# Kernel optimization log

Measured on AMD Instinct MI355X. Metric: run time of the kernel, lower is better.

Reference implementation:

```python
import jax, jax.numpy as jnp
import numpy as np

N_NODES = 50000
N_EDGES = 800000
N_GRAPHS = 512
EPS = 1e-5
SLOPE = 0.2  # LeakyReLU negative slope in GATv2


def setup_inputs() -> dict:
    key = jax.random.key(0)
    ks = jax.random.split(key, 20)
    s = 0.1
    inp = {
        "x": jax.random.normal(ks[0], (N_NODES, 9), jnp.float32),
        "edge_attr": jax.random.normal(ks[1], (N_EDGES, 3), jnp.float32),
        "Wl0": jax.random.normal(ks[2], (9, 64), jnp.float32) * s,
        "Wr0": jax.random.normal(ks[3], (9, 64), jnp.float32) * s,
        "bl0": jnp.zeros((64,), jnp.float32),
        "br0": jnp.zeros((64,), jnp.float32),
        "We0": jax.random.normal(ks[4], (3, 64), jnp.float32) * s,
        "att0": jax.random.normal(ks[5], (64,), jnp.float32) * s,
        "bo0": jnp.zeros((64,), jnp.float32),
        "Wl": jax.random.normal(ks[6], (4, 64, 64), jnp.float32) * s,
        "Wr": jax.random.normal(ks[7], (4, 64, 64), jnp.float32) * s,
        "bl": jnp.zeros((4, 64), jnp.float32),
        "br": jnp.zeros((4, 64), jnp.float32),
        "We": jax.random.normal(ks[8], (4, 3, 64), jnp.float32) * s,
        "att": jax.random.normal(ks[9], (4, 64), jnp.float32) * s,
        "bo": jnp.zeros((4, 64), jnp.float32),
        "bn_g": jnp.ones((5, 64), jnp.float32),
        "bn_b": jnp.zeros((5, 64), jnp.float32),
        "bn_m": jnp.zeros((5, 64), jnp.float32),
        "bn_v": jax.random.uniform(ks[10], (5, 64), jnp.float32, 0.5, 1.5),
        "Wjk": jax.random.normal(ks[11], (64, 64), jnp.float32) * s,
        "bjk": jnp.zeros((64,), jnp.float32),
        "Whead": jax.random.normal(ks[12], (64, 1), jnp.float32) * s,
        "bhead": jnp.zeros((1,), jnp.float32),
        "edge_index": jax.random.randint(ks[13], (2, N_EDGES), 0, N_NODES, jnp.int32),
        "batch": jnp.sort(jax.random.randint(ks[14], (N_NODES,), 0, N_GRAPHS, jnp.int32)),
        "num_graphs": N_GRAPHS,
    }
    return inp


def gatv2_layer(h, src, dst, ea, Wl_, bl_, Wr_, br_, We_, a_, bo_, n_nodes):
    # GATv2Conv (heads=1, edge_dim) : e_ij = a . LeakyReLU(Wl h_j + Wr h_i + We e_ij)
    xl = h @ Wl_ + bl_                          # [N, 64] source transform
    xr = h @ Wr_ + br_                          # [N, 64] dest transform
    e = jax.nn.leaky_relu(xl[src] + xr[dst] + ea @ We_, SLOPE)  # [E, 64]
    logit = e @ a_                              # [E]
    m = jax.ops.segment_max(logit, dst, num_segments=n_nodes)
    m = jnp.where(jnp.isfinite(m), m, 0.0)      # empty segments -> -inf
    p = jnp.exp(logit - m[dst])
    z = jax.ops.segment_sum(p, dst, num_segments=n_nodes)
    alpha = p / jnp.maximum(z[dst], 1e-16)      # softmax over in-edges of dst
    out = jax.ops.segment_sum(alpha[:, None] * xl[src], dst, num_segments=n_nodes)
    return out + bo_


def bn_relu(h, g, b, m, v):
    # eval-mode BatchNorm1d followed by ReLU (BasicGNN: norm then act)
    return jax.nn.relu((h - m) * (g * jax.lax.rsqrt(v + EPS)) + b)


def reference(x, edge_attr, Wl0, Wr0, bl0, br0, We0, att0, bo0,
              Wl, Wr, bl, br, We, att, bo,
              bn_g, bn_b, bn_m, bn_v, Wjk, bjk, Whead, bhead,
              edge_index, batch, num_graphs):
    n = x.shape[0]
    src, dst = edge_index[0], edge_index[1]
    h = gatv2_layer(x, src, dst, edge_attr, Wl0, bl0, Wr0, br0, We0, att0, bo0, n)
    h = bn_relu(h, bn_g[0], bn_b[0], bn_m[0], bn_v[0])
    for i in range(4):
        h = gatv2_layer(h, src, dst, edge_attr, Wl[i], bl[i], Wr[i], br[i], We[i], att[i], bo[i], n)
        h = bn_relu(h, bn_g[i + 1], bn_b[i + 1], bn_m[i + 1], bn_v[i + 1])
    h = h @ Wjk + bjk                            # jk='last' output projection 64->64
    # global mean pool over graphs
    sums = jax.ops.segment_sum(h, batch, num_segments=num_graphs)          # [G, 64]
    cnt = jax.ops.segment_sum(jnp.ones((n,), h.dtype), batch, num_segments=num_graphs)
    pooled = sums / jnp.maximum(cnt, 1.0)[:, None]
    return pooled @ Whead + bhead                # [G, 1]  (dropout inactive in eval)
```

## Files before the change

### kernel.cpp

```cpp
#include <hip/hip_runtime.h>
#include <math.h>

#define N_NODES 50000
#define N_EDGES 800000
#define N_GRAPHS 512
#define SLOPE 0.2f
#define CAP 48
static constexpr float EPS_BN = 1e-5f;

typedef float v2f __attribute__((ext_vector_type(2)));


__global__ __launch_bounds__(256) void scatter_t9_kernel(
    const int* __restrict__ src, const int* __restrict__ dst,
    const float* __restrict__ ea,
    int* __restrict__ cnt, float4* __restrict__ rec,
    const float* __restrict__ x,
    const float* __restrict__ Wl0, const float* __restrict__ bl0,
    const float* __restrict__ Wr0, const float* __restrict__ br0,
    float* __restrict__ xl, float* __restrict__ xr) {
    int t = threadIdx.x;
    int e = blockIdx.x * 256 + t;
    if (e < N_EDGES) {
        int d = dst[e];
        int pos = atomicAdd(&cnt[d], 1);
        if (pos < CAP)
            rec[(size_t)d * CAP + pos] = make_float4(__int_as_float(src[e] * 64),
                                                     ea[e * 3 + 0], ea[e * 3 + 1], ea[e * 3 + 2]);
    }

    int w = t >> 6;
    int k = t & 63;
    v2f wlr[9];
#pragma unroll
    for (int j = 0; j < 9; j++) wlr[j] = (v2f){Wl0[j * 64 + k], Wr0[j * 64 + k]};
    v2f bias = {bl0[k], br0[k]};
    const int NW = gridDim.x * 4;
    for (int n = blockIdx.x * 4 + w; n < N_NODES; n += NW) {
        int un = __builtin_amdgcn_readfirstlane(n);
        const float* __restrict__ hrow = x + (size_t)un * 9;
        float hb[9];
#pragma unroll
        for (int j = 0; j < 9; j++) hb[j] = hrow[j];
        v2f acc = bias;
#pragma unroll
        for (int j = 0; j < 9; j++)
            acc = __builtin_elementwise_fma((v2f){hb[j], hb[j]}, wlr[j], acc);
        xl[(size_t)un * 64 + k] = acc.x;
        xr[(size_t)un * 64 + k] = acc.y;
    }
}


__global__ __launch_bounds__(256) void transform5_kernel(
    const float* __restrict__ h,
    const float* __restrict__ Wl, const float* __restrict__ bl,
    const float* __restrict__ Wr, const float* __restrict__ br,
    float* __restrict__ xl, float* __restrict__ xr) {
    __shared__ float sAt[64][68];
    __shared__ float sB[64][128];
    int t = threadIdx.x;
    int n0 = blockIdx.x * 64;

#pragma unroll
    for (int i = 0; i < 4; i++) {
        int idx = i * 256 + t;
        int row = idx >> 4;
        int fc  = idx & 15;
        int n = n0 + row;
        float4 v = (n < N_NODES) ? *((const float4*)(h + (size_t)n * 64 + fc * 4))
                                 : make_float4(0.f, 0.f, 0.f, 0.f);
        sAt[fc * 4 + 0][row] = v.x;
        sAt[fc * 4 + 1][row] = v.y;
        sAt[fc * 4 + 2][row] = v.z;
        sAt[fc * 4 + 3][row] = v.w;
    }
#pragma unroll
    for (int i = 0; i < 8; i++) {
        int idx = i * 256 + t;
        int j  = idx >> 5;
        int fc = idx & 31;
        int c  = fc * 4;
        float4 v = (c < 64) ? *((const float4*)(Wl + j * 64 + c))
                            : *((const float4*)(Wr + j * 64 + (c - 64)));
        *((float4*)&sB[j][c]) = v;
    }
    __syncthreads();

    int tx = t & 15, ty = t >> 4;
    int col0 = tx * 8;
    const float* bsrc = (col0 < 64) ? (bl + col0) : (br + (col0 - 64));
    v2f acc[4][4];
#pragma unroll
    for (int r = 0; r < 4; r++)
#pragma unroll
        for (int cc = 0; cc < 4; cc++)
            acc[r][cc] = (v2f){bsrc[cc * 2], bsrc[cc * 2 + 1]};

#pragma unroll 4
    for (int j = 0; j < 64; j++) {
        float a0 = sAt[j][ty * 4 + 0];
        float a1 = sAt[j][ty * 4 + 1];
        float a2 = sAt[j][ty * 4 + 2];
        float a3 = sAt[j][ty * 4 + 3];
        float4 bq0 = *((const float4*)&sB[j][col0]);
        float4 bq1 = *((const float4*)&sB[j][col0 + 4]);
        v2f b0 = {bq0.x, bq0.y}, b1 = {bq0.z, bq0.w};
        v2f b2 = {bq1.x, bq1.y}, b3 = {bq1.z, bq1.w};
        v2f a0v = {a0, a0}, a1v = {a1, a1}, a2v = {a2, a2}, a3v = {a3, a3};
        acc[0][0] = __builtin_elementwise_fma(a0v, b0, acc[0][0]);
        acc[0][1] = __builtin_elementwise_fma(a0v, b1, acc[0][1]);
        acc[0][2] = __builtin_elementwise_fma(a0v, b2, acc[0][2]);
        acc[0][3] = __builtin_elementwise_fma(a0v, b3, acc[0][3]);
        acc[1][0] = __builtin_elementwise_fma(a1v, b0, acc[1][0]);
        acc[1][1] = __builtin_elementwise_fma(a1v, b1, acc[1][1]);
        acc[1][2] = __builtin_elementwise_fma(a1v, b2, acc[1][2]);
        acc[1][3] = __builtin_elementwise_fma(a1v, b3, acc[1][3]);
        acc[2][0] = __builtin_elementwise_fma(a2v, b0, acc[2][0]);
        acc[2][1] = __builtin_elementwise_fma(a2v, b1, acc[2][1]);
        acc[2][2] = __builtin_elementwise_fma(a2v, b2, acc[2][2]);
        acc[2][3] = __builtin_elementwise_fma(a2v, b3, acc[2][3]);
        acc[3][0] = __builtin_elementwise_fma(a3v, b0, acc[3][0]);
        acc[3][1] = __builtin_elementwise_fma(a3v, b1, acc[3][1]);
        acc[3][2] = __builtin_elementwise_fma(a3v, b2, acc[3][2]);
        acc[3][3] = __builtin_elementwise_fma(a3v, b3, acc[3][3]);
    }

#pragma unroll
    for (int r = 0; r < 4; r++) {
        int n = n0 + ty * 4 + r;
        if (n < N_NODES) {
            float4 lo = make_float4(acc[r][0].x, acc[r][0].y, acc[r][1].x, acc[r][1].y);
            float4 hi = make_float4(acc[r][2].x, acc[r][2].y, acc[r][3].x, acc[r][3].y);
            float* dstp = (col0 < 64) ? (xl + (size_t)n * 64 + col0)
                                      : (xr + (size_t)n * 64 + (col0 - 64));
            *((float4*)dstp) = lo;
            *((float4*)(dstp + 4)) = hi;
        }
    }
}


#define GAT_BODY(MASKED)                                                             \
    {                                                                                \
        int pA = c + q;                                                              \
        int pB = c + 4 + q;                                                          \
        bool vA = true, vB = true;                                                   \
        if (MASKED) {                                                                \
            vA = pA < end; if (!vA) pA = beg;                                        \
            vB = pB < end; if (!vB) pB = beg;                                        \
        }                                                                            \
        float4 rA = recP[pA];                                                        \
        float4 rB = recP[pB];                                                        \
        unsigned offA = (unsigned)__float_as_int(rA.x) + k4;                         \
        unsigned offB = (unsigned)__float_as_int(rB.x) + k4;                         \
        float4 xA = *(const float4*)(xl + offA);                                     \
        float4 xB = *(const float4*)(xl + offB);                                     \
        v2f xAa = {xA.x, xA.y}, xAb = {xA.z, xA.w};                                  \
        v2f xBa = {xB.x, xB.y}, xBb = {xB.z, xB.w};                                  \
        v2f tAa = xAa + xra, tAb = xAb + xrb;                                        \
        v2f tBa = xBa + xra, tBb = xBb + xrb;                                        \
        tAa = __builtin_elementwise_fma((v2f){rA.y, rA.y}, we0a, tAa);               \
        tAb = __builtin_elementwise_fma((v2f){rA.y, rA.y}, we0b, tAb);               \
        tBa = __builtin_elementwise_fma((v2f){rB.y, rB.y}, we0a, tBa);               \
        tBb = __builtin_elementwise_fma((v2f){rB.y, rB.y}, we0b, tBb);               \
        tAa = __builtin_elementwise_fma((v2f){rA.z, rA.z}, we1a, tAa);               \
        tAb = __builtin_elementwise_fma((v2f){rA.z, rA.z}, we1b, tAb);               \
        tBa = __builtin_elementwise_fma((v2f){rB.z, rB.z}, we1a, tBa);               \
        tBb = __builtin_elementwise_fma((v2f){rB.z, rB.z}, we1b, tBb);               \
        tAa = __builtin_elementwise_fma((v2f){rA.w, rA.w}, we2a, tAa);               \
        tAb = __builtin_elementwise_fma((v2f){rA.w, rA.w}, we2b, tAb);               \
        tBa = __builtin_elementwise_fma((v2f){rB.w, rB.w}, we2a, tBa);               \
        tBb = __builtin_elementwise_fma((v2f){rB.w, rB.w}, we2b, tBb);               \
        tAa = __builtin_elementwise_max(tAa, tAa * SLOPE);                           \
        tAb = __builtin_elementwise_max(tAb, tAb * SLOPE);                           \
        tBa = __builtin_elementwise_max(tBa, tBa * SLOPE);                           \
        tBb = __builtin_elementwise_max(tBb, tBb * SLOPE);                           \
        v2f dA = ata * tAa; dA = __builtin_elementwise_fma(atb, tAb, dA);            \
        v2f dB = ata * tBa; dB = __builtin_elementwise_fma(atb, tBb, dB);            \
        float accA = dA.x + dA.y;                                                    \
        float accB = dB.x + dB.y;                                                    \
        accA += __shfl_xor(accA, 1, 64);  accB += __shfl_xor(accB, 1, 64);           \
        accA += __shfl_xor(accA, 2, 64);  accB += __shfl_xor(accB, 2, 64);           \
        accA += __shfl_xor(accA, 4, 64);  accB += __shfl_xor(accB, 4, 64);           \
        accA += __shfl_xor(accA, 8, 64);  accB += __shfl_xor(accB, 8, 64);           \
        float peA = __expf(accA);                                                    \
        float peB = __expf(accB);                                                    \
        if (MASKED) { peA = vA ? peA : 0.f; peB = vB ? peB : 0.f; }                  \
        v2f pA2 = {peA, peA}, pB2 = {peB, peB};                                      \
        oAa = __builtin_elementwise_fma(pA2, xAa, oAa);                              \
        oAb = __builtin_elementwise_fma(pA2, xAb, oAb);                              \
        oBa = __builtin_elementwise_fma(pB2, xBa, oBa);                              \
        oBb = __builtin_elementwise_fma(pB2, xBb, oBb);                              \
        zA += peA; zB += peB;                                                        \
    }

__global__ __launch_bounds__(256) void gat_fused8_kernel(
    const float* __restrict__ xl, const float* __restrict__ xr,
    const float4* __restrict__ recP, const int* __restrict__ cnt,
    const float* __restrict__ We, const float* __restrict__ att,
    const float* __restrict__ bo,
    const float* __restrict__ bn_g, const float* __restrict__ bn_b,
    const float* __restrict__ bn_m, const float* __restrict__ bn_v,
    float* __restrict__ hout) {
    int t = threadIdx.x;
    int w = t >> 6;
    int lane = t & 63;
    int q = lane >> 4;
    int r = lane & 15;
    int k4 = r * 4;

    float4 we0 = *(const float4*)(We + 0 * 64 + k4);
    float4 we1 = *(const float4*)(We + 64 + k4);
    float4 we2 = *(const float4*)(We + 128 + k4);
    float4 at4 = *(const float4*)(att + k4);
    v2f we0a = {we0.x, we0.y}, we0b = {we0.z, we0.w};
    v2f we1a = {we1.x, we1.y}, we1b = {we1.z, we1.w};
    v2f we2a = {we2.x, we2.y}, we2b = {we2.z, we2.w};
    v2f ata  = {at4.x, at4.y}, atb  = {at4.z, at4.w};

    float4 g4  = *(const float4*)(bn_g + k4);
    float4 b4  = *(const float4*)(bn_b + k4);
    float4 m4  = *(const float4*)(bn_m + k4);
    float4 v4  = *(const float4*)(bn_v + k4);
    float4 bo4 = *(const float4*)(bo + k4);
    float Sx = g4.x * rsqrtf(v4.x + EPS_BN);
    float Sy = g4.y * rsqrtf(v4.y + EPS_BN);
    float Sz = g4.z * rsqrtf(v4.z + EPS_BN);
    float Sw = g4.w * rsqrtf(v4.w + EPS_BN);
    v2f Sa = {Sx, Sy}, Sb = {Sz, Sw};
    v2f Ta = {fmaf(bo4.x - m4.x, Sx, b4.x), fmaf(bo4.y - m4.y, Sy, b4.y)};
    v2f Tb = {fmaf(bo4.z - m4.z, Sz, b4.z), fmaf(bo4.w - m4.w, Sw, b4.w)};

    int n0 = blockIdx.x * 8 + w * 2;

#pragma unroll
    for (int nn = 0; nn < 2; nn++) {
        int n = n0 + nn;
        float4 xq = *(const float4*)(xr + (size_t)n * 64 + k4);
        v2f xra = {xq.x, xq.y}, xrb = {xq.z, xq.w};
        int deg = min(cnt[n], CAP);
        int beg = n * CAP;
        int end = beg + deg;
        int fullc = beg + (deg & ~7);

        v2f oAa = {0.f, 0.f}, oAb = {0.f, 0.f};
        v2f oBa = {0.f, 0.f}, oBb = {0.f, 0.f};
        float zA = 0.f, zB = 0.f;

        int c = beg;
        for (; c < fullc; c += 8) GAT_BODY(0)
        if (c < end) GAT_BODY(1)

        v2f oa = oAa + oBa, ob = oAb + oBb;
        float z = zA + zB;
        float4 o = make_float4(oa.x, oa.y, ob.x, ob.y);
        o.x += __shfl_xor(o.x, 16, 64); o.x += __shfl_xor(o.x, 32, 64);
        o.y += __shfl_xor(o.y, 16, 64); o.y += __shfl_xor(o.y, 32, 64);
        o.z += __shfl_xor(o.z, 16, 64); o.z += __shfl_xor(o.z, 32, 64);
        o.w += __shfl_xor(o.w, 16, 64); o.w += __shfl_xor(o.w, 32, 64);
        z += __shfl_xor(z, 16, 64); z += __shfl_xor(z, 32, 64);

        if (q == 0) {
            float zi = __builtin_amdgcn_rcpf(fmaxf(z, 1e-16f));
            v2f ra = {o.x * zi, o.y * zi};
            v2f rb = {o.z * zi, o.w * zi};
            ra = __builtin_elementwise_fma(ra, Sa, Ta);
            rb = __builtin_elementwise_fma(rb, Sb, Tb);
            ra = __builtin_elementwise_max(ra, (v2f){0.f, 0.f});
            rb = __builtin_elementwise_max(rb, (v2f){0.f, 0.f});
            float4 res = make_float4(ra.x, ra.y, rb.x, rb.y);
            *(float4*)(hout + (size_t)n * 64 + k4) = res;
        }
    }
}


__global__ __launch_bounds__(64) void pool_all_kernel(
    const float* __restrict__ h, const int* __restrict__ batch,
    const float* __restrict__ Wjk, const float* __restrict__ bjk,
    const float* __restrict__ Whead, const float* __restrict__ bhead,
    float* __restrict__ out) {
    int g = blockIdx.x;
    int k = threadIdx.x;
    int lo = 0, hi = N_NODES;
    while (lo < hi) { int mid = (lo + hi) >> 1; if (batch[mid] < g) lo = mid + 1; else hi = mid; }
    int s = lo;
    hi = N_NODES;
    while (lo < hi) { int mid = (lo + hi) >> 1; if (batch[mid] < g + 1) lo = mid + 1; else hi = mid; }
    int e = lo;

    float wc = 0.f;
    for (int j = 0; j < 64; j++) wc = fmaf(Wjk[k * 64 + j], Whead[j], wc);
    float bc = bjk[k] * Whead[k];
    for (int off = 32; off > 0; off >>= 1) bc += __shfl_xor(bc, off, 64);

    float acc = 0.f;
    for (int n = s; n < e; ++n) acc += h[(size_t)n * 64 + k];
    float cntf = (float)(e - s);
    acc /= fmaxf(cntf, 1.0f);
    float v = acc * wc;
    for (int off = 32; off > 0; off >>= 1) v += __shfl_xor(v, off, 64);
    if (k == 0) out[g] = v + bc + bhead[0];
}


extern "C" void kernel_launch(void* const* d_in, const int* in_sizes, int n_in,
                              void* d_out, int out_size, void* d_ws, size_t ws_size,
                              hipStream_t stream) {
    const float* x     = (const float*)d_in[0];
    const float* ea    = (const float*)d_in[1];
    const float* Wl0   = (const float*)d_in[2];
    const float* Wr0   = (const float*)d_in[3];
    const float* bl0   = (const float*)d_in[4];
    const float* br0   = (const float*)d_in[5];
    const float* We0   = (const float*)d_in[6];
    const float* att0  = (const float*)d_in[7];
    const float* bo0   = (const float*)d_in[8];
    const float* Wl    = (const float*)d_in[9];
    const float* Wr    = (const float*)d_in[10];
    const float* bl    = (const float*)d_in[11];
    const float* br    = (const float*)d_in[12];
    const float* We    = (const float*)d_in[13];
    const float* att   = (const float*)d_in[14];
    const float* bo    = (const float*)d_in[15];
    const float* bn_g  = (const float*)d_in[16];
    const float* bn_b  = (const float*)d_in[17];
    const float* bn_m  = (const float*)d_in[18];
    const float* bn_v  = (const float*)d_in[19];
    const float* Wjk   = (const float*)d_in[20];
    const float* bjk   = (const float*)d_in[21];
    const float* Whead = (const float*)d_in[22];
    const float* bhead = (const float*)d_in[23];
    const int* edge_index = (const int*)d_in[24];
    const int* batch      = (const int*)d_in[25];

    const int* srcIdx = edge_index;
    const int* dstIdx = edge_index + N_EDGES;

    char* ws = (char*)d_ws;
    size_t off = 0;
    auto alloc = [&](size_t bytes) -> void* {
        void* p = ws + off;
        off += (bytes + 255) & ~(size_t)255;
        return p;
    };
    float* hA      = (float*)alloc((size_t)N_NODES * 64 * 4);
    float* hB      = (float*)alloc((size_t)N_NODES * 64 * 4);
    float* xlb     = (float*)alloc((size_t)N_NODES * 64 * 4);
    float* xrb     = (float*)alloc((size_t)N_NODES * 64 * 4);
    int*   cnt     = (int*)alloc((size_t)N_NODES * 4);
    float4* recP   = (float4*)alloc((size_t)N_NODES * CAP * 16);

    hipMemsetAsync(cnt, 0, (size_t)N_NODES * 4, stream);
    scatter_t9_kernel<<<(N_EDGES + 255) / 256, 256, 0, stream>>>(
        srcIdx, dstIdx, ea, cnt, recP, x, Wl0, bl0, Wr0, br0, xlb, xrb);

    const int NBN2 = N_NODES / 8;
    const int NBG  = (N_NODES + 63) / 64;

    gat_fused8_kernel<<<NBN2, 256, 0, stream>>>(xlb, xrb, recP, cnt,
                                                We0, att0, bo0,
                                                bn_g, bn_b, bn_m, bn_v, hA);

    float* hcur = hA;
    float* hnext = hB;
    for (int i = 0; i < 4; i++) {
        transform5_kernel<<<NBG, 256, 0, stream>>>(hcur,
            Wl + (size_t)i * 64 * 64, bl + (size_t)i * 64,
            Wr + (size_t)i * 64 * 64, br + (size_t)i * 64,
            xlb, xrb);
        gat_fused8_kernel<<<NBN2, 256, 0, stream>>>(xlb, xrb, recP, cnt,
            We + (size_t)i * 3 * 64, att + (size_t)i * 64,
            bo + (size_t)i * 64,
            bn_g + (size_t)(i + 1) * 64, bn_b + (size_t)(i + 1) * 64,
            bn_m + (size_t)(i + 1) * 64, bn_v + (size_t)(i + 1) * 64,
            hnext);
        float* tp = hcur; hcur = hnext; hnext = tp;
    }

    pool_all_kernel<<<N_GRAPHS, 64, 0, stream>>>(hcur, batch, Wjk, bjk, Whead, bhead,
                                                 (float*)d_out);
}
```

Before: 531.3 us.

## Fuse GAT aggregation with next layer's linear transform in one kernel

Replaces the separate transform and GAT aggregation kernels with a layer-fused kernel. Each 1024-thread block aggregates 64 nodes, applies BN+ReLU into shared memory, then immediately computes the next layer's Wl/Wr projections, so the hidden state never round-trips through global memory. The masked tail loop is also merged into a single predicated loop, and BN scale/shift is recomputed with a division and sqrt instead of precomputed rsqrt constants. The risks are lower occupancy and more serialized work per block, since each wave processes four nodes sequentially in the 1024-thread blocks.

```diff
diff --git a/kernel.cpp b/kernel.cpp
--- a/kernel.cpp
+++ b/kernel.cpp
@@ -52,106 +52,15 @@
 }
 
 
-__global__ __launch_bounds__(256) void transform5_kernel(
-    const float* __restrict__ h,
-    const float* __restrict__ Wl, const float* __restrict__ bl,
-    const float* __restrict__ Wr, const float* __restrict__ br,
-    float* __restrict__ xl, float* __restrict__ xr) {
-    __shared__ float sAt[64][68];
-    __shared__ float sB[64][128];
-    int t = threadIdx.x;
-    int n0 = blockIdx.x * 64;
-
-#pragma unroll
-    for (int i = 0; i < 4; i++) {
-        int idx = i * 256 + t;
-        int row = idx >> 4;
-        int fc  = idx & 15;
-        int n = n0 + row;
-        float4 v = (n < N_NODES) ? *((const float4*)(h + (size_t)n * 64 + fc * 4))
-                                 : make_float4(0.f, 0.f, 0.f, 0.f);
-        sAt[fc * 4 + 0][row] = v.x;
-        sAt[fc * 4 + 1][row] = v.y;
-        sAt[fc * 4 + 2][row] = v.z;
-        sAt[fc * 4 + 3][row] = v.w;
-    }
-#pragma unroll
-    for (int i = 0; i < 8; i++) {
-        int idx = i * 256 + t;
-        int j  = idx >> 5;
-        int fc = idx & 31;
-        int c  = fc * 4;
-        float4 v = (c < 64) ? *((const float4*)(Wl + j * 64 + c))
-                            : *((const float4*)(Wr + j * 64 + (c - 64)));
-        *((float4*)&sB[j][c]) = v;
-    }
-    __syncthreads();
-
-    int tx = t & 15, ty = t >> 4;
-    int col0 = tx * 8;
-    const float* bsrc = (col0 < 64) ? (bl + col0) : (br + (col0 - 64));
-    v2f acc[4][4];
-#pragma unroll
-    for (int r = 0; r < 4; r++)
-#pragma unroll
-        for (int cc = 0; cc < 4; cc++)
-            acc[r][cc] = (v2f){bsrc[cc * 2], bsrc[cc * 2 + 1]};
-
-#pragma unroll 4
-    for (int j = 0; j < 64; j++) {
-        float a0 = sAt[j][ty * 4 + 0];
-        float a1 = sAt[j][ty * 4 + 1];
-        float a2 = sAt[j][ty * 4 + 2];
-        float a3 = sAt[j][ty * 4 + 3];
-        float4 bq0 = *((const float4*)&sB[j][col0]);
-        float4 bq1 = *((const float4*)&sB[j][col0 + 4]);
-        v2f b0 = {bq0.x, bq0.y}, b1 = {bq0.z, bq0.w};
-        v2f b2 = {bq1.x, bq1.y}, b3 = {bq1.z, bq1.w};
-        v2f a0v = {a0, a0}, a1v = {a1, a1}, a2v = {a2, a2}, a3v = {a3, a3};
-        acc[0][0] = __builtin_elementwise_fma(a0v, b0, acc[0][0]);
-        acc[0][1] = __builtin_elementwise_fma(a0v, b1, acc[0][1]);
-        acc[0][2] = __builtin_elementwise_fma(a0v, b2, acc[0][2]);
-        acc[0][3] = __builtin_elementwise_fma(a0v, b3, acc[0][3]);
-        acc[1][0] = __builtin_elementwise_fma(a1v, b0, acc[1][0]);
-        acc[1][1] = __builtin_elementwise_fma(a1v, b1, acc[1][1]);
-        acc[1][2] = __builtin_elementwise_fma(a1v, b2, acc[1][2]);
-        acc[1][3] = __builtin_elementwise_fma(a1v, b3, acc[1][3]);
-        acc[2][0] = __builtin_elementwise_fma(a2v, b0, acc[2][0]);
-        acc[2][1] = __builtin_elementwise_fma(a2v, b1, acc[2][1]);
-        acc[2][2] = __builtin_elementwise_fma(a2v, b2, acc[2][2]);
-        acc[2][3] = __builtin_elementwise_fma(a2v, b3, acc[2][3]);
-        acc[3][0] = __builtin_elementwise_fma(a3v, b0, acc[3][0]);
-        acc[3][1] = __builtin_elementwise_fma(a3v, b1, acc[3][1]);
-        acc[3][2] = __builtin_elementwise_fma(a3v, b2, acc[3][2]);
-        acc[3][3] = __builtin_elementwise_fma(a3v, b3, acc[3][3]);
-    }
-
-#pragma unroll
-    for (int r = 0; r < 4; r++) {
-        int n = n0 + ty * 4 + r;
-        if (n < N_NODES) {
-            float4 lo = make_float4(acc[r][0].x, acc[r][0].y, acc[r][1].x, acc[r][1].y);
-            float4 hi = make_float4(acc[r][2].x, acc[r][2].y, acc[r][3].x, acc[r][3].y);
-            float* dstp = (col0 < 64) ? (xl + (size_t)n * 64 + col0)
-                                      : (xr + (size_t)n * 64 + (col0 - 64));
-            *((float4*)dstp) = lo;
-            *((float4*)(dstp + 4)) = hi;
-        }
-    }
-}
-
-
-#define GAT_BODY(MASKED)                                                             \
-    {                                                                                \
-        int pA = c + q;                                                              \
-        int pB = c + 4 + q;                                                          \
-        bool vA = true, vB = true;                                                   \
-        if (MASKED) {                                                                \
-            vA = pA < end; if (!vA) pA = beg;                                        \
-            vB = pB < end; if (!vB) pB = beg;                                        \
-        }                                                                            \
-        float4 rA = recP[pA];                                                        \
-        float4 rB = recP[pB];                                                        \
+#define GAT_EDGE_LOOP()                                                              \
+    v2f oAa = {0.f, 0.f}, oAb = {0.f, 0.f};                                          \
+    v2f oBa = {0.f, 0.f}, oBb = {0.f, 0.f};                                          \
+    float zA = 0.f, zB = 0.f;                                                        \
+    for (int c = beg; c < end; c += 8) {                                             \
+        int pA = c + q;     bool vA = pA < end; int iA = vA ? pA : beg;              \
+        int pB = c + 4 + q; bool vB = pB < end; int iB = vB ? pB : beg;              \
+        float4 rA = recP[iA];                                                        \
+        float4 rB = recP[iB];                                                        \
         unsigned offA = (unsigned)__float_as_int(rA.x) + k4;                         \
         unsigned offB = (unsigned)__float_as_int(rB.x) + k4;                         \
         float4 xA = *(const float4*)(xl + offA);                                     \
@@ -184,18 +93,146 @@
         accA += __shfl_xor(accA, 2, 64);  accB += __shfl_xor(accB, 2, 64);           \
         accA += __shfl_xor(accA, 4, 64);  accB += __shfl_xor(accB, 4, 64);           \
         accA += __shfl_xor(accA, 8, 64);  accB += __shfl_xor(accB, 8, 64);           \
-        float peA = __expf(accA);                                                    \
-        float peB = __expf(accB);                                                    \
-        if (MASKED) { peA = vA ? peA : 0.f; peB = vB ? peB : 0.f; }                  \
+        float peA = vA ? __expf(accA) : 0.f;                                         \
+        float peB = vB ? __expf(accB) : 0.f;                                         \
         v2f pA2 = {peA, peA}, pB2 = {peB, peB};                                      \
         oAa = __builtin_elementwise_fma(pA2, xAa, oAa);                              \
         oAb = __builtin_elementwise_fma(pA2, xAb, oAb);                              \
         oBa = __builtin_elementwise_fma(pB2, xBa, oBa);                              \
         oBb = __builtin_elementwise_fma(pB2, xBb, oBb);                              \
         zA += peA; zB += peB;                                                        \
-    }
-
-__global__ __launch_bounds__(256) void gat_fused8_kernel(
+    }                                                                                \
+    v2f oa = oAa + oBa, ob = oAb + oBb;                                              \
+    float z = zA + zB;                                                               \
+    float4 o = make_float4(oa.x, oa.y, ob.x, ob.y);                                  \
+    o.x += __shfl_xor(o.x, 16, 64); o.x += __shfl_xor(o.x, 32, 64);                  \
+    o.y += __shfl_xor(o.y, 16, 64); o.y += __shfl_xor(o.y, 32, 64);                  \
+    o.z += __shfl_xor(o.z, 16, 64); o.z += __shfl_xor(o.z, 32, 64);                  \
+    o.w += __shfl_xor(o.w, 16, 64); o.w += __shfl_xor(o.w, 32, 64);                  \
+    z += __shfl_xor(z, 16, 64); z += __shfl_xor(z, 32, 64);
+
+#define GAT_PROLOGUE()                                                               \
+    float4 we0 = *(const float4*)(We + 0 * 64 + k4);                                 \
+    float4 we1 = *(const float4*)(We + 64 + k4);                                     \
+    float4 we2 = *(const float4*)(We + 128 + k4);                                    \
+    float4 at4 = *(const float4*)(att + k4);                                         \
+    v2f we0a = {we0.x, we0.y}, we0b = {we0.z, we0.w};                                \
+    v2f we1a = {we1.x, we1.y}, we1b = {we1.z, we1.w};                                \
+    v2f we2a = {we2.x, we2.y}, we2b = {we2.z, we2.w};                                \
+    v2f ata  = {at4.x, at4.y}, atb  = {at4.z, at4.w};                                \
+    float4 bo4 = *(const float4*)(bo + k4);                                          \
+    float4 g4  = *(const float4*)(bn_g + k4);                                        \
+    float4 b4  = *(const float4*)(bn_b + k4);                                        \
+    float4 m4  = *(const float4*)(bn_m + k4);                                        \
+    float4 v4  = *(const float4*)(bn_v + k4);
+
+#define GAT_BN_RES()                                                                 \
+    float zi = 1.0f / fmaxf(z, 1e-16f);                                              \
+    float4 res;                                                                      \
+    res.x = fmaxf((o.x * zi + bo4.x - m4.x) * (g4.x / sqrtf(v4.x + EPS_BN)) + b4.x, 0.f); \
+    res.y = fmaxf((o.y * zi + bo4.y - m4.y) * (g4.y / sqrtf(v4.y + EPS_BN)) + b4.y, 0.f); \
+    res.z = fmaxf((o.z * zi + bo4.z - m4.z) * (g4.z / sqrtf(v4.z + EPS_BN)) + b4.z, 0.f); \
+    res.w = fmaxf((o.w * zi + bo4.w - m4.w) * (g4.w / sqrtf(v4.w + EPS_BN)) + b4.w, 0.f);
+
+
+__global__ __launch_bounds__(1024) void layer_fused_kernel(
+    const float* __restrict__ xl, const float* __restrict__ xr,
+    const float4* __restrict__ recP, const int* __restrict__ cnt,
+    const float* __restrict__ We, const float* __restrict__ att,
+    const float* __restrict__ bo,
+    const float* __restrict__ bn_g, const float* __restrict__ bn_b,
+    const float* __restrict__ bn_m, const float* __restrict__ bn_v,
+    const float* __restrict__ Wl, const float* __restrict__ bl,
+    const float* __restrict__ Wr, const float* __restrict__ br,
+    float* __restrict__ xl_out, float* __restrict__ xr_out) {
+    __shared__ float sAt[64][65];
+    __shared__ float sB[64][128];
+    int t = threadIdx.x;
+    int n0 = blockIdx.x * 64;
+
+#pragma unroll
+    for (int i = 0; i < 2; i++) {
+        int idx = i * 1024 + t;
+        int j  = idx >> 5;
+        int fc = idx & 31;
+        int c  = fc * 4;
+        float4 v = (c < 64) ? *((const float4*)(Wl + j * 64 + c))
+                            : *((const float4*)(Wr + j * 64 + (c - 64)));
+        *((float4*)&sB[j][c]) = v;
+    }
+
+    int w = t >> 6;
+    int lane = t & 63;
+    int q = lane >> 4;
+    int r = lane & 15;
+    int k4 = r * 4;
+
+    GAT_PROLOGUE()
+
+#pragma unroll
+    for (int nn = 0; nn < 4; nn++) {
+        int nb = w * 4 + nn;
+        int n = n0 + nb;
+        if (n < N_NODES) {
+            float4 xq = *(const float4*)(xr + (size_t)n * 64 + k4);
+            v2f xra = {xq.x, xq.y}, xrb = {xq.z, xq.w};
+            int beg = n * CAP;
+            int end = beg + min(cnt[n], CAP);
+            GAT_EDGE_LOOP()
+            if (q == 0) {
+                GAT_BN_RES()
+                sAt[k4 + 0][nb] = res.x;
+                sAt[k4 + 1][nb] = res.y;
+                sAt[k4 + 2][nb] = res.z;
+                sAt[k4 + 3][nb] = res.w;
+            }
+        } else if (q == 0) {
+            sAt[k4 + 0][nb] = 0.f;
+            sAt[k4 + 1][nb] = 0.f;
+            sAt[k4 + 2][nb] = 0.f;
+            sAt[k4 + 3][nb] = 0.f;
+        }
+    }
+    __syncthreads();
+
+    int tx = t & 63;
+    int ty = t >> 6;
+    int col0 = tx * 2;
+    const float* bsrc = (col0 < 64) ? (bl + col0) : (br + (col0 - 64));
+    v2f bias = {bsrc[0], bsrc[1]};
+    v2f a0 = bias, a1 = bias, a2 = bias, a3 = bias;
+    int row0 = ty * 4;
+#pragma unroll 8
+    for (int j = 0; j < 64; j++) {
+        float h0 = sAt[j][row0 + 0];
+        float h1 = sAt[j][row0 + 1];
+        float h2 = sAt[j][row0 + 2];
+        float h3 = sAt[j][row0 + 3];
+        v2f b = *((const v2f*)&sB[j][col0]);
+        a0 = __builtin_elementwise_fma((v2f){h0, h0}, b, a0);
+        a1 = __builtin_elementwise_fma((v2f){h1, h1}, b, a1);
+        a2 = __builtin_elementwise_fma((v2f){h2, h2}, b, a2);
+        a3 = __builtin_elementwise_fma((v2f){h3, h3}, b, a3);
+    }
+    float* outbase = (col0 < 64) ? (xl_out + col0) : (xr_out + (col0 - 64));
+    {
+        int n = n0 + row0;
+        if (n + 3 < N_NODES) {
+            *((v2f*)(outbase + (size_t)(n + 0) * 64)) = a0;
+            *((v2f*)(outbase + (size_t)(n + 1) * 64)) = a1;
+            *((v2f*)(outbase + (size_t)(n + 2) * 64)) = a2;
+            *((v2f*)(outbase + (size_t)(n + 3) * 64)) = a3;
+        } else {
+            if (n + 0 < N_NODES) *((v2f*)(outbase + (size_t)(n + 0) * 64)) = a0;
+            if (n + 1 < N_NODES) *((v2f*)(outbase + (size_t)(n + 1) * 64)) = a1;
+            if (n + 2 < N_NODES) *((v2f*)(outbase + (size_t)(n + 2) * 64)) = a2;
+            if (n + 3 < N_NODES) *((v2f*)(outbase + (size_t)(n + 3) * 64)) = a3;
+        }
+    }
+}
+
+
+__global__ __launch_bounds__(256) void gat_final_kernel(
     const float* __restrict__ xl, const float* __restrict__ xr,
     const float4* __restrict__ recP, const int* __restrict__ cnt,
     const float* __restrict__ We, const float* __restrict__ att,
@@ -209,69 +246,17 @@
     int q = lane >> 4;
     int r = lane & 15;
     int k4 = r * 4;
-
-    float4 we0 = *(const float4*)(We + 0 * 64 + k4);
-    float4 we1 = *(const float4*)(We + 64 + k4);
-    float4 we2 = *(const float4*)(We + 128 + k4);
-    float4 at4 = *(const float4*)(att + k4);
-    v2f we0a = {we0.x, we0.y}, we0b = {we0.z, we0.w};
-    v2f we1a = {we1.x, we1.y}, we1b = {we1.z, we1.w};
-    v2f we2a = {we2.x, we2.y}, we2b = {we2.z, we2.w};
-    v2f ata  = {at4.x, at4.y}, atb  = {at4.z, at4.w};
-
-    float4 g4  = *(const float4*)(bn_g + k4);
-    float4 b4  = *(const float4*)(bn_b + k4);
-    float4 m4  = *(const float4*)(bn_m + k4);
-    float4 v4  = *(const float4*)(bn_v + k4);
-    float4 bo4 = *(const float4*)(bo + k4);
-    float Sx = g4.x * rsqrtf(v4.x + EPS_BN);
-    float Sy = g4.y * rsqrtf(v4.y + EPS_BN);
-    float Sz = g4.z * rsqrtf(v4.z + EPS_BN);
-    float Sw = g4.w * rsqrtf(v4.w + EPS_BN);
-    v2f Sa = {Sx, Sy}, Sb = {Sz, Sw};
-    v2f Ta = {fmaf(bo4.x - m4.x, Sx, b4.x), fmaf(bo4.y - m4.y, Sy, b4.y)};
-    v2f Tb = {fmaf(bo4.z - m4.z, Sz, b4.z), fmaf(bo4.w - m4.w, Sw, b4.w)};
-
-    int n0 = blockIdx.x * 8 + w * 2;
-
-#pragma unroll
-    for (int nn = 0; nn < 2; nn++) {
-        int n = n0 + nn;
-        float4 xq = *(const float4*)(xr + (size_t)n * 64 + k4);
-        v2f xra = {xq.x, xq.y}, xrb = {xq.z, xq.w};
-        int deg = min(cnt[n], CAP);
-        int beg = n * CAP;
-        int end = beg + deg;
-        int fullc = beg + (deg & ~7);
-
-        v2f oAa = {0.f, 0.f}, oAb = {0.f, 0.f};
-        v2f oBa = {0.f, 0.f}, oBb = {0.f, 0.f};
-        float zA = 0.f, zB = 0.f;
-
-        int c = beg;
-        for (; c < fullc; c += 8) GAT_BODY(0)
-        if (c < end) GAT_BODY(1)
-
-        v2f oa = oAa + oBa, ob = oAb + oBb;
-        float z = zA + zB;
-        float4 o = make_float4(oa.x, oa.y, ob.x, ob.y);
-        o.x += __shfl_xor(o.x, 16, 64); o.x += __shfl_xor(o.x, 32, 64);
-        o.y += __shfl_xor(o.y, 16, 64); o.y += __shfl_xor(o.y, 32, 64);
-        o.z += __shfl_xor(o.z, 16, 64); o.z += __shfl_xor(o.z, 32, 64);
-        o.w += __shfl_xor(o.w, 16, 64); o.w += __shfl_xor(o.w, 32, 64);
-        z += __shfl_xor(z, 16, 64); z += __shfl_xor(z, 32, 64);
-
-        if (q == 0) {
-            float zi = __builtin_amdgcn_rcpf(fmaxf(z, 1e-16f));
-            v2f ra = {o.x * zi, o.y * zi};
-            v2f rb = {o.z * zi, o.w * zi};
-            ra = __builtin_elementwise_fma(ra, Sa, Ta);
-            rb = __builtin_elementwise_fma(rb, Sb, Tb);
-            ra = __builtin_elementwise_max(ra, (v2f){0.f, 0.f});
-            rb = __builtin_elementwise_max(rb, (v2f){0.f, 0.f});
-            float4 res = make_float4(ra.x, ra.y, rb.x, rb.y);
-            *(float4*)(hout + (size_t)n * 64 + k4) = res;
-        }
+    int n = blockIdx.x * 4 + w;
+
+    GAT_PROLOGUE()
+    float4 xq = *(const float4*)(xr + (size_t)n * 64 + k4);
+    v2f xra = {xq.x, xq.y}, xrb = {xq.z, xq.w};
+    int beg = n * CAP;
+    int end = beg + min(cnt[n], CAP);
+    GAT_EDGE_LOOP()
+    if (q == 0) {
+        GAT_BN_RES()
+        *(float4*)(hout + (size_t)n * 64 + k4) = res;
     }
 }
 
@@ -345,40 +330,50 @@
         off += (bytes + 255) & ~(size_t)255;
         return p;
     };
-    float* hA      = (float*)alloc((size_t)N_NODES * 64 * 4);
-    float* hB      = (float*)alloc((size_t)N_NODES * 64 * 4);
-    float* xlb     = (float*)alloc((size_t)N_NODES * 64 * 4);
-    float* xrb     = (float*)alloc((size_t)N_NODES * 64 * 4);
+    float* xlA     = (float*)alloc((size_t)N_NODES * 64 * 4);
+    float* xrA     = (float*)alloc((size_t)N_NODES * 64 * 4);
+    float* xlB     = (float*)alloc((size_t)N_NODES * 64 * 4);
+    float* xrB     = (float*)alloc((size_t)N_NODES * 64 * 4);
+    float* hfin    = (float*)alloc((size_t)N_NODES * 64 * 4);
     int*   cnt     = (int*)alloc((size_t)N_NODES * 4);
     float4* recP   = (float4*)alloc((size_t)N_NODES * CAP * 16);
 
     hipMemsetAsync(cnt, 0, (size_t)N_NODES * 4, stream);
     scatter_t9_kernel<<<(N_EDGES + 255) / 256, 256, 0, stream>>>(
-        srcIdx, dstIdx, ea, cnt, recP, x, Wl0, bl0, Wr0, br0, xlb, xrb);
-
-    const int NBN2 = N_NODES / 8;
-    const int NBG  = (N_NODES + 63) / 64;
-
-    gat_fused8_kernel<<<NBN2, 256, 0, stream>>>(xlb, xrb, recP, cnt,
-                                                We0, att0, bo0,
-                                                bn_g, bn_b, bn_m, bn_v, hA);
-
-    float* hcur = hA;
-    float* hnext = hB;
-    for (int i = 0; i < 4; i++) {
-        transform5_kernel<<<NBG, 256, 0, stream>>>(hcur,
-            Wl + (size_t)i * 64 * 64, bl + (size_t)i * 64,
-            Wr + (size_t)i * 64 * 64, br + (size_t)i * 64,
-            xlb, xrb);
-        gat_fused8_kernel<<<NBN2, 256, 0, stream>>>(xlb, xrb, recP, cnt,
-            We + (size_t)i * 3 * 64, att + (size_t)i * 64,
-            bo + (size_t)i * 64,
-            bn_g + (size_t)(i + 1) * 64, bn_b + (size_t)(i + 1) * 64,
-            bn_m + (size_t)(i + 1) * 64, bn_v + (size_t)(i + 1) * 64,
-            hnext);
-        float* tp = hcur; hcur = hnext; hnext = tp;
-    }
-
-    pool_all_kernel<<<N_GRAPHS, 64, 0, stream>>>(hcur, batch, Wjk, bjk, Whead, bhead,
+        srcIdx, dstIdx, ea, cnt, recP, x, Wl0, bl0, Wr0, br0, xlA, xrA);
+
+    const int NBF = (N_NODES + 63) / 64;
+    const int NBN = N_NODES / 4;
+
+    layer_fused_kernel<<<NBF, 1024, 0, stream>>>(
+        xlA, xrA, recP, cnt, We0, att0, bo0,
+        bn_g, bn_b, bn_m, bn_v,
+        Wl, bl, Wr, br, xlB, xrB);
+    const float* xin[2][2] = {{xlA, xrA}, {xlB, xrB}};
+    for (int L = 1; L < 4; L++) {
+        const float* inl = (L & 1) ? xlB : xlA;
+        const float* inr = (L & 1) ? xrB : xrA;
+        float* outl = (L & 1) ? xlA : xlB;
+        float* outr = (L & 1) ? xrA : xrB;
+        layer_fused_kernel<<<NBF, 1024, 0, stream>>>(
+            inl, inr, recP, cnt,
+            We + (size_t)(L - 1) * 3 * 64, att + (size_t)(L - 1) * 64,
+            bo + (size_t)(L - 1) * 64,
+            bn_g + (size_t)L * 64, bn_b + (size_t)L * 64,
+            bn_m + (size_t)L * 64, bn_v + (size_t)L * 64,
+            Wl + (size_t)L * 64 * 64, bl + (size_t)L * 64,
+            Wr + (size_t)L * 64 * 64, br + (size_t)L * 64,
+            outl, outr);
+    }
+    (void)xin;
+
+    gat_final_kernel<<<NBN, 256, 0, stream>>>(
+        xlA, xrA, recP, cnt,
+        We + (size_t)3 * 3 * 64, att + (size_t)3 * 64, bo + (size_t)3 * 64,
+        bn_g + (size_t)4 * 64, bn_b + (size_t)4 * 64,
+        bn_m + (size_t)4 * 64, bn_v + (size_t)4 * 64,
+        hfin);
+
+    pool_all_kernel<<<N_GRAPHS, 64, 0, stream>>>(hfin, batch, Wjk, bjk, Whead, bhead,
                                                  (float*)d_out);
 }
```

Result: slower. 582.8 us (+9.7%).
